# Kernel tuning notes

Measured on AMD Instinct MI355X. Metric: run time of the kernel, lower is better.

## Reference

```python
import jax, jax.numpy as jnp
from jax import lax
import numpy as np

# Config matching init_kwargs
NUM_CLASSES = 19
K = 200               # keep_k_centers
NMS_KERNEL = 9
CENTER_THR = 0.1
LABEL_DIV = 256
VOID = 255
STUFF_AREA = 4096
THING_IDS = np.array([11, 12, 13, 14, 15, 16, 17, 18])
IS_THING = jnp.zeros(NUM_CLASSES, bool).at[jnp.asarray(THING_IDS)].set(True)


def _process_one(logits, heat, offset):
    # logits [C,H,W], heat [1,H,W], offset [2,H,W]
    C, H, W = logits.shape
    sem = jnp.argmax(logits, axis=0).astype(jnp.int32)          # [H,W]
    h = heat[0]
    ht = jnp.where(h > CENTER_THR, h, 0.0)
    pad = NMS_KERNEL // 2
    # torch max_pool2d pads implicitly with -inf
    pooled = lax.reduce_window(ht, -jnp.inf, lax.max,
                               (NMS_KERNEL, NMS_KERNEL), (1, 1),
                               ((pad, pad), (pad, pad)))
    nms = jnp.where(ht == pooled, ht, 0.0)                      # [H,W]
    flat = nms.reshape(-1)
    scores, idx = lax.top_k(flat, K)                            # fixed-size center set
    valid = scores > 0.0
    num_pos = jnp.sum(flat > 0.0)
    # Match torch ordering: if more than K peaks -> topk (descending-score) order;
    # otherwise nonzero() row-major order. Invalid slots pushed to the end.
    big = jnp.int32(H * W + K)
    order_key = jnp.where(valid,
                          jnp.where(num_pos > K,
                                    jnp.arange(K, dtype=jnp.int32),
                                    idx.astype(jnp.int32)),
                          big)
    perm = jnp.argsort(order_key)
    idx = idx[perm]
    valid = valid[perm]
    FAR = 1e9  # invalid centers placed infinitely far away
    cy = jnp.where(valid, (idx // W).astype(jnp.float32), FAR)
    cx = jnp.where(valid, (idx % W).astype(jnp.float32), FAR)
    ty = jnp.arange(H, dtype=jnp.float32)[:, None] + offset[0]  # [H,W]
    tx = jnp.arange(W, dtype=jnp.float32)[None, :] + offset[1]  # [H,W]
    # squared distances [H,W,K]; argmin equals argmin of cdist
    d2 = (ty[..., None] - cy) ** 2 + (tx[..., None] - cx) ** 2
    closest = jnp.argmin(d2, axis=-1).astype(jnp.int32)         # [H,W]
    thing_mask = IS_THING[sem]
    inst = jnp.where(thing_mask & valid.any(), closest + 1, 0).astype(jnp.int32)
    # Majority class per instance via (instance, class) histogram.
    # argmax picks the smallest class among ties, matching torch.mode.
    hist = jnp.zeros((K + 1) * NUM_CLASSES, jnp.int32)
    hist = hist.at[(inst * NUM_CLASSES + sem).reshape(-1)].add(1)
    hist = hist.reshape(K + 1, NUM_CLASSES)
    majority = jnp.argmax(hist, axis=1).astype(jnp.int32)       # [K+1]
    pan = jnp.where(inst > 0, majority[inst] * LABEL_DIV + inst, VOID * LABEL_DIV)
    # Stuff: per-class pixel counts restricted to non-instance pixels
    stuff_pix = inst == 0
    skey = jnp.where(stuff_pix, sem, NUM_CLASSES).reshape(-1)
    scounts = jnp.zeros(NUM_CLASSES + 1, jnp.int32).at[skey].add(1)[:NUM_CLASSES]
    cond = stuff_pix & (~thing_mask) & (scounts[sem] >= STUFF_AREA)
    pan = jnp.where(cond, sem * LABEL_DIV, pan)
    return pan.astype(jnp.int32), inst


def setup_inputs() -> dict:
    key = jax.random.key(0)
    k1, k2, k3 = jax.random.split(key, 3)
    B, C, H, W = 2, NUM_CLASSES, 512, 1024
    semantic_logits = jax.random.normal(k1, (B, C, H, W), dtype=jnp.float32)
    center_heatmap = jax.random.uniform(k2, (B, 1, H, W), dtype=jnp.float32)
    offset_map = jax.random.normal(k3, (B, 2, H, W), dtype=jnp.float32)
    return {"semantic_logits": semantic_logits,
            "center_heatmap": center_heatmap,
            "offset_map": offset_map}


def reference(semantic_logits, center_heatmap, offset_map):
    pan, inst = jax.vmap(_process_one)(semantic_logits, center_heatmap, offset_map)
    return pan, inst
```

## Files before the change

### kernel.cpp

```cpp
#include <hip/hip_runtime.h>

#define B 2
#define C 19
#define H 512
#define W 1024
#define HW (H*W)
#define K 200
#define NCLS 19
#define HISTN ((K+1)*NCLS)
#define NT 512
#define MAXPB 128
#define SL 6912

typedef unsigned long long u64;


__global__ __launch_bounds__(256) void k_nms(const float* __restrict__ heat,
                                             u64* __restrict__ keys,
                                             int* __restrict__ pcnt) {
    __shared__ float ht[40][40];
    __shared__ float hm[40][32];
    __shared__ u64 lpk[MAXPB];
    __shared__ int lcnt;
    int b = blockIdx.z;
    int x0 = blockIdx.x * 32, y0 = blockIdx.y * 32;
    int gb = b * NT + blockIdx.y * 32 + blockIdx.x;
    int tid = threadIdx.y * 32 + threadIdx.x;
    const float* hb = heat + (size_t)b * HW;
    if (tid == 0) lcnt = 0;
    for (int i = tid; i < 40 * 40; i += 256) {
        int ly = i / 40, lx = i % 40;
        int gy = y0 + ly - 4, gx = x0 + lx - 4;
        float v = 0.f;
        if (gy >= 0 && gy < H && gx >= 0 && gx < W) {
            float hv = hb[gy * W + gx];
            v = (hv > 0.1f) ? hv : 0.f;
        }
        ht[ly][lx] = v;
    }
    __syncthreads();
    for (int i = tid; i < 40 * 32; i += 256) {
        int ly = i >> 5, lx = i & 31;
        float m = ht[ly][lx];
#pragma unroll
        for (int d = 1; d < 9; ++d) m = fmaxf(m, ht[ly][lx + d]);
        hm[ly][lx] = m;
    }
    __syncthreads();
#pragma unroll
    for (int r = 0; r < 4; ++r) {
        int oy = threadIdx.y + r * 8;
        int ox = threadIdx.x;
        float c = ht[oy + 4][ox + 4];
        if (c > 0.f) {
            float m = hm[oy][ox];
#pragma unroll
            for (int d = 1; d < 9; ++d) m = fmaxf(m, hm[oy + d][ox]);
            if (c == m) {
                int pos = atomicAdd(&lcnt, 1);
                unsigned sb = __float_as_uint(c);
                if (pos < MAXPB)
                    lpk[pos] = ((u64)(0x3F800000u - sb) << 19)
                             | (unsigned)((y0 + oy) * W + (x0 + ox));
            }
        }
    }
    __syncthreads();
    int n = (lcnt < MAXPB) ? lcnt : MAXPB;
    if (tid == 0) pcnt[gb] = n;
    for (int i = tid; i < n; i += 256)
        keys[(size_t)gb * MAXPB + i] = lpk[i];
}

__global__ __launch_bounds__(1024) void k_topk(const u64* __restrict__ keys,
                                               const int* __restrict__ pcnt,
                                               int* __restrict__ hist,
                                               int* __restrict__ anyv,
                                               float* __restrict__ cy,
                                               float* __restrict__ cx) {
    __shared__ u64 skeys[SL];
    __shared__ u64 cand[256];
    __shared__ int hcnt[256];
    __shared__ int sbase[NT], scnt[NT];
    __shared__ int wsum[16];
    __shared__ u64 s_thr;
    __shared__ int sR, gcnt, s_binc;
    int b = blockIdx.x, tid = threadIdx.x;
    int lane = tid & 63, w = tid >> 6;
    for (int i = tid; i < HISTN; i += 1024) hist[b * HISTN + i] = 0;
    int n = (tid < NT) ? pcnt[b * NT + tid] : 0;
    int incl = n;
#pragma unroll
    for (int off = 1; off < 64; off <<= 1) {
        int v = __shfl_up(incl, off, 64);
        if (lane >= off) incl += v;
    }
    if (tid < NT && lane == 63) wsum[w] = incl;
    __syncthreads();
    int N = 0;
#pragma unroll
    for (int j = 0; j < 8; ++j) N += wsum[j];
    if (tid < NT) {
        int wbase = 0;
        for (int j = 0; j < w; ++j) wbase += wsum[j];
        sbase[tid] = wbase + incl - n;
        scnt[tid] = n;
    }
    int M = (N < SL) ? N : SL;
    int Ksel = (M < K) ? M : K;
    if (tid == 0) { s_thr = 0ULL; sR = Ksel; gcnt = 0; s_binc = 0x7FFFFFFF; }
    __syncthreads();
    for (int t = w * 32; t < w * 32 + 32; ++t) {
        int nt_ = scnt[t];
        if (lane < nt_) {
            int d = sbase[t] + lane;
            if (d < SL)
                skeys[d] = keys[(size_t)(b * NT + t) * MAXPB + lane];
        }
    }
    __syncthreads();
    u64 thr;
    if (M <= K) {
        thr = ~0ULL;
    } else {
        bool donep = false;
#pragma unroll 1
        for (int d = 40; d >= 0 && !donep; d -= 8) {
            if (tid < 256) hcnt[tid] = 0;
            __syncthreads();
            u64 pref = s_thr;
            for (int i = tid; i < M; i += 1024) {
                u64 kk = skeys[i];
                if ((kk >> (d + 8)) == (pref >> (d + 8)))
                    atomicAdd(&hcnt[(int)((kk >> d) & 255ULL)], 1);
            }
            __syncthreads();
            if (tid < 64) {
                int h0 = hcnt[tid * 4 + 0], h1 = hcnt[tid * 4 + 1];
                int h2 = hcnt[tid * 4 + 2], h3 = hcnt[tid * 4 + 3];
                int s = h0 + h1 + h2 + h3;
                int ic = s;
#pragma unroll
                for (int off = 1; off < 64; off <<= 1) {
                    int v = __shfl_up(ic, off, 64);
                    if (tid >= off) ic += v;
                }
                int R = sR;
                int before = ic - s;
                if (before < R && R <= ic) {
                    int c = before, t = tid * 4;
                    if (c + h0 < R) { c += h0; t++;
                        if (c + h1 < R) { c += h1; t++;
                            if (c + h2 < R) { c += h2; t++; } } }
                    s_thr = pref | ((u64)t << d);
                    sR = R - c;
                    s_binc = hcnt[t];
                }
            }
            __syncthreads();
            if (s_binc <= 256) {
                u64 p2 = s_thr;
                for (int i = tid; i < M; i += 1024) {
                    u64 kk = skeys[i];
                    if ((kk >> d) == (p2 >> d)) {
                        int p = atomicAdd(&gcnt, 1);
                        if (p < 256) cand[p] = kk;
                    }
                }
                __syncthreads();
                int g = (gcnt < 256) ? gcnt : 256;
                if (tid < g) {
                    u64 v = cand[tid];
                    int r = 0;
                    for (int j = 0; j < g; ++j) r += (int)(cand[j] < v);
                    if (r == sR - 1) s_thr = v;
                }
                __syncthreads();
                if (tid == 0) gcnt = 0;
                donep = true;
                __syncthreads();
            }
        }
        thr = s_thr;
    }
    for (int i = tid; i < M; i += 1024) {
        u64 kk = skeys[i];
        if (kk <= thr) {
            int p = atomicAdd(&gcnt, 1);
            if (p < 256) cand[p] = kk;
        }
    }
    __syncthreads();
    if (tid < 256) {
        int g = (gcnt < 256) ? gcnt : 256;
        u64 v = (tid < g) ? cand[tid] : ~0ULL;
        if (N <= K && tid < g) v &= 0x7FFFFULL;
        cand[tid] = v;
    }
    __syncthreads();
    if (tid < 256) {
        u64 v = cand[tid];
        int r = 0;
#pragma unroll 8
        for (int j = 0; j < 256; ++j) {
            u64 cj = cand[j];
            r += (int)((cj < v) || (cj == v && j < tid));
        }
        skeys[r] = v;
    }
    __syncthreads();
    if (tid < K) {
        bool valid = tid < Ksel;
        unsigned idx = (unsigned)(skeys[tid] & 0x7FFFFULL);
        cy[b * K + tid] = valid ? (float)(idx >> 10) : 1e9f;
        cx[b * K + tid] = valid ? (float)(idx & 1023) : 1e9f;
    }
    if (tid == 0) anyv[b] = (N > 0) ? 1 : 0;
}

__global__ __launch_bounds__(256) void k_inst(const float* __restrict__ logits,
                                              const float* __restrict__ offs,
                                              const float* __restrict__ gcy,
                                              const float* __restrict__ gcx,
                                              const int* __restrict__ anyv,
                                              int* __restrict__ packed,
                                              int* __restrict__ hist) {
    __shared__ int lh[HISTN];
    __shared__ float scy[K], scx[K];
    __shared__ unsigned char skk[K];
    __shared__ float red[4][8];
    __shared__ int wcnt[4];
    int b = blockIdx.z;
    int x0 = blockIdx.x << 5, y0 = blockIdx.y << 5;
    int tid = threadIdx.x;
    int lane = tid & 63, w = tid >> 6;
    for (int i = tid; i < HISTN; i += 256) lh[i] = 0;
    int r = tid >> 3;
    int c0 = (tid & 7) << 2;
    int gy = y0 + r;
    int gxb = x0 + c0;
    int q = (gy << 10) + gxb;
    const float* ob = offs + (size_t)b * 2 * HW;
    float4 oy4 = *(const float4*)(ob + q);
    float4 ox4 = *(const float4*)(ob + HW + q);
    int av = anyv[b];
    const float4* l4 = (const float4*)(logits + (size_t)b * C * HW) + (q >> 2);
    float4 vv[C];
#pragma unroll
    for (int c = 0; c < C; ++c) vv[c] = l4[(size_t)c * (HW / 4)];
    float fy = (float)gy, fx = (float)gxb;
    float ty[4] = {fy + oy4.x, fy + oy4.y, fy + oy4.z, fy + oy4.w};
    float tx[4] = {fx + ox4.x, fx + 1.f + ox4.y, fx + 2.f + ox4.z, fx + 3.f + ox4.w};
    float tylo = fminf(fminf(ty[0], ty[1]), fminf(ty[2], ty[3]));
    float tyhi = fmaxf(fmaxf(ty[0], ty[1]), fmaxf(ty[2], ty[3]));
    float txlo = fminf(fminf(tx[0], tx[1]), fminf(tx[2], tx[3]));
    float txhi = fmaxf(fmaxf(tx[0], tx[1]), fmaxf(tx[2], tx[3]));
#pragma unroll
    for (int off = 32; off; off >>= 1) {
        tylo = fminf(tylo, __shfl_xor(tylo, off, 64));
        tyhi = fmaxf(tyhi, __shfl_xor(tyhi, off, 64));
        txlo = fminf(txlo, __shfl_xor(txlo, off, 64));
        txhi = fmaxf(txhi, __shfl_xor(txhi, off, 64));
    }
    if (lane == 0) { red[w][0] = tylo; red[w][1] = tyhi; red[w][2] = txlo; red[w][3] = txhi; }
    __syncthreads();
    tylo = fminf(fminf(red[0][0], red[1][0]), fminf(red[2][0], red[3][0]));
    tyhi = fmaxf(fmaxf(red[0][1], red[1][1]), fmaxf(red[2][1], red[3][1]));
    txlo = fminf(fminf(red[0][2], red[1][2]), fminf(red[2][2], red[3][2]));
    txhi = fmaxf(fmaxf(red[0][3], red[1][3]), fmaxf(red[2][3], red[3][3]));
    float kcy = 0.f, kcx = 0.f, mind2 = 0.f, maxd2 = 3.4e38f;
    if (tid < K) {
        kcy = gcy[b * K + tid]; kcx = gcx[b * K + tid];
        float dmy = fmaxf(fmaxf(tylo - kcy, kcy - tyhi), 0.f);
        float dMy = fmaxf(tyhi - kcy, kcy - tylo);
        float dmx = fmaxf(fmaxf(txlo - kcx, kcx - txhi), 0.f);
        float dMx = fmaxf(txhi - kcx, kcx - txlo);
        mind2 = dmy * dmy + dmx * dmx;
        maxd2 = dMy * dMy + dMx * dMx;
    }
    float mv = maxd2;
#pragma unroll
    for (int off = 32; off; off >>= 1) mv = fminf(mv, __shfl_xor(mv, off, 64));
    if (lane == 0) red[w][4] = mv;
    __syncthreads();
    float m = fminf(fminf(red[0][4], red[1][4]), fminf(red[2][4], red[3][4]));
    bool keep = (tid < K) && (mind2 <= m * 1.0001f + 1.0f);
    u64 bal = __ballot(keep);
    if (lane == 0) wcnt[w] = (int)__popcll(bal);
    __syncthreads();
    int nk = wcnt[0] + wcnt[1] + wcnt[2] + wcnt[3];
    if (keep) {
        int base = (w > 0 ? wcnt[0] : 0) + (w > 1 ? wcnt[1] : 0) + (w > 2 ? wcnt[2] : 0);
        int rank = base + (int)__popcll(bal & ((1ULL << lane) - 1ULL));
        scy[rank] = kcy; scx[rank] = kcx; skk[rank] = (unsigned char)tid;
    }
    float best[4] = {vv[0].x, vv[0].y, vv[0].z, vv[0].w};
    int bc[4] = {0, 0, 0, 0};
#pragma unroll
    for (int c = 1; c < C; ++c) {
        if (vv[c].x > best[0]) { best[0] = vv[c].x; bc[0] = c; }
        if (vv[c].y > best[1]) { best[1] = vv[c].y; bc[1] = c; }
        if (vv[c].z > best[2]) { best[2] = vv[c].z; bc[2] = c; }
        if (vv[c].w > best[3]) { best[3] = vv[c].w; bc[3] = c; }
    }
    __syncthreads();
    float bd[4] = {3.4e38f, 3.4e38f, 3.4e38f, 3.4e38f};
    int bi[4] = {0, 0, 0, 0};
    if (av) {
        for (int i = 0; i < nk; ++i) {
            float cyk = scy[i], cxk = scx[i];
#pragma unroll
            for (int j = 0; j < 4; ++j) {
                float dy = __fsub_rn(ty[j], cyk);
                float dx = __fsub_rn(tx[j], cxk);
                float d2 = __fadd_rn(__fmul_rn(dy, dy), __fmul_rn(dx, dx));
                if (d2 < bd[j]) { bd[j] = d2; bi[j] = i; }
            }
        }
    }
    int4 pk4;
    int* pkp = (int*)&pk4;
#pragma unroll
    for (int j = 0; j < 4; ++j) {
        int s = bc[j];
        int ins = (s >= 11 && av) ? ((int)skk[bi[j]] + 1) : 0;
        pkp[j] = (s << 8) | ins;
        atomicAdd(&lh[ins * NCLS + s], 1);
    }
    *(int4*)(packed + b * HW + q) = pk4;
    __syncthreads();
    for (int i = tid; i < HISTN; i += 256)
        if (lh[i]) atomicAdd(&hist[b * HISTN + i], lh[i]);
}

__global__ __launch_bounds__(256) void k_pan(int* __restrict__ pansem,
                                             int* __restrict__ inst,
                                             const int* __restrict__ hist) {
    __shared__ int lh[HISTN];
    __shared__ unsigned char maj[K + 1];
    int b = blockIdx.x >> 8;
    int blk = blockIdx.x & 255;
    int tid = threadIdx.x;
    const int* hb = hist + b * HISTN;
    for (int i = tid; i < HISTN; i += 256) lh[i] = hb[i];
    __syncthreads();
    if (tid <= K) {
        const int* h = &lh[tid * NCLS];
        int best = h[0], bc = 0;
#pragma unroll
        for (int c = 1; c < NCLS; ++c)
            if (h[c] > best) { best = h[c]; bc = c; }
        maj[tid] = (unsigned char)bc;
    }
    __syncthreads();
    int p0 = b * HW + blk * 2048;
    const int4* s4 = (const int4*)(pansem + p0);
    int4 pka = s4[tid * 2], pkb = s4[tid * 2 + 1];
    int4 pa, pb, ia, ib;
    int* kp = (int*)&pka; int* pp = (int*)&pa; int* ip = (int*)&ia;
#pragma unroll
    for (int j = 0; j < 4; ++j) {
        int s = kp[j] >> 8, in_ = kp[j] & 255;
        pp[j] = (in_ > 0) ? ((int)maj[in_] * 256 + in_)
               : ((s < 11 && lh[s] >= 4096) ? s * 256 : 65280);
        ip[j] = in_;
    }
    kp = (int*)&pkb; pp = (int*)&pb; ip = (int*)&ib;
#pragma unroll
    for (int j = 0; j < 4; ++j) {
        int s = kp[j] >> 8, in_ = kp[j] & 255;
        pp[j] = (in_ > 0) ? ((int)maj[in_] * 256 + in_)
               : ((s < 11 && lh[s] >= 4096) ? s * 256 : 65280);
        ip[j] = in_;
    }
    ((int4*)(pansem + p0))[tid * 2] = pa;
    ((int4*)(pansem + p0))[tid * 2 + 1] = pb;
    ((int4*)(inst + p0))[tid * 2] = ia;
    ((int4*)(inst + p0))[tid * 2 + 1] = ib;
}

extern "C" void kernel_launch(void* const* d_in, const int* in_sizes, int n_in,
                              void* d_out, int out_size, void* d_ws, size_t ws_size,
                              hipStream_t stream) {
    const float* logits = (const float*)d_in[0];
    const float* heat   = (const float*)d_in[1];
    const float* offs   = (const float*)d_in[2];
    int* out = (int*)d_out;
    int* pansem = out;
    int* inst = out + B * HW;
    int* wsi = (int*)d_ws;
    int* hist = wsi + 16;
    float* cy = (float*)(wsi + 8192);
    float* cx = cy + B * K;
    int* pcnt = wsi + 9216;
    int* anyv = wsi + 10496;
    u64* keys = (u64*)((char*)d_ws + 65536);

    k_nms<<<dim3(32, 16, B), dim3(32, 8, 1), 0, stream>>>(heat, keys, pcnt);
    k_topk<<<B, 1024, 0, stream>>>(keys, pcnt, hist, anyv, cy, cx);
    k_inst<<<dim3(32, 16, B), 256, 0, stream>>>(logits, offs, cy, cx, anyv, pansem, hist);
    k_pan<<<B * 256, 256, 0, stream>>>(pansem, inst, hist);
}
```

Before: 75.52 us.

## Shrink k_inst tiles to 32x16 and restructure top-k key gather

The instance kernel now has each thread handle 2 pixels instead of 4 and covers 32x16 tiles, which doubles the grid. The aim is more blocks in flight and lower register pressure, and the smaller tiles should also give tighter center-pruning bounds. In exchange, the per-block pruning and histogram-flush overhead doubles. Separately, MAXPB drops from 128 to 64 peaks per NMS tile, and the top-k gather uses one prefix array with strided tile ownership per wave. A tile with more than 64 peaks would now be truncated.

Measured after the change: 83.50 us. 1.11x slower.

```diff
diff --git a/kernel.cpp b/kernel.cpp
--- a/kernel.cpp
+++ b/kernel.cpp
@@ -9,7 +9,7 @@
 #define NCLS 19
 #define HISTN ((K+1)*NCLS)
 #define NT 512
-#define MAXPB 128
+#define MAXPB 64
 #define SL 6912
 
 typedef unsigned long long u64;
@@ -81,8 +81,8 @@
     __shared__ u64 skeys[SL];
     __shared__ u64 cand[256];
     __shared__ int hcnt[256];
-    __shared__ int sbase[NT], scnt[NT];
-    __shared__ int wsum[16];
+    __shared__ int sbase[NT + 1];
+    __shared__ int wsum[8];
     __shared__ u64 s_thr;
     __shared__ int sR, gcnt, s_binc;
     int b = blockIdx.x, tid = threadIdx.x;
@@ -104,18 +104,23 @@
         int wbase = 0;
         for (int j = 0; j < w; ++j) wbase += wsum[j];
         sbase[tid] = wbase + incl - n;
-        scnt[tid] = n;
+        if (tid == NT - 1) sbase[NT] = N;
     }
     int M = (N < SL) ? N : SL;
     int Ksel = (M < K) ? M : K;
     if (tid == 0) { s_thr = 0ULL; sR = Ksel; gcnt = 0; s_binc = 0x7FFFFFFF; }
     __syncthreads();
-    for (int t = w * 32; t < w * 32 + 32; ++t) {
-        int nt_ = scnt[t];
-        if (lane < nt_) {
-            int d = sbase[t] + lane;
-            if (d < SL)
-                skeys[d] = keys[(size_t)(b * NT + t) * MAXPB + lane];
+    {
+        int t = w;
+        const u64* kb = keys + (size_t)b * NT * MAXPB;
+#pragma unroll 1
+        for (int it = 0; it < NT / 16; ++it, t += 16) {
+            int base = sbase[t];
+            int cnt_ = sbase[t + 1] - base;
+            if (lane < cnt_) {
+                int d = base + lane;
+                if (d < SL) skeys[d] = kb[(size_t)t * MAXPB + lane];
+            }
         }
     }
     __syncthreads();
@@ -231,30 +236,28 @@
     __shared__ float red[4][8];
     __shared__ int wcnt[4];
     int b = blockIdx.z;
-    int x0 = blockIdx.x << 5, y0 = blockIdx.y << 5;
+    int x0 = blockIdx.x << 5, y0 = blockIdx.y << 4;
     int tid = threadIdx.x;
     int lane = tid & 63, w = tid >> 6;
     for (int i = tid; i < HISTN; i += 256) lh[i] = 0;
-    int r = tid >> 3;
-    int c0 = (tid & 7) << 2;
+    int r = tid >> 4;
+    int c0 = (tid & 15) << 1;
     int gy = y0 + r;
     int gxb = x0 + c0;
     int q = (gy << 10) + gxb;
     const float* ob = offs + (size_t)b * 2 * HW;
-    float4 oy4 = *(const float4*)(ob + q);
-    float4 ox4 = *(const float4*)(ob + HW + q);
+    float2 oy2 = *(const float2*)(ob + q);
+    float2 ox2 = *(const float2*)(ob + HW + q);
     int av = anyv[b];
-    const float4* l4 = (const float4*)(logits + (size_t)b * C * HW) + (q >> 2);
-    float4 vv[C];
-#pragma unroll
-    for (int c = 0; c < C; ++c) vv[c] = l4[(size_t)c * (HW / 4)];
+    const float2* l2 = (const float2*)(logits + (size_t)b * C * HW) + (q >> 1);
+    float2 vv[C];
+#pragma unroll
+    for (int c = 0; c < C; ++c) vv[c] = l2[(size_t)c * (HW / 2)];
     float fy = (float)gy, fx = (float)gxb;
-    float ty[4] = {fy + oy4.x, fy + oy4.y, fy + oy4.z, fy + oy4.w};
-    float tx[4] = {fx + ox4.x, fx + 1.f + ox4.y, fx + 2.f + ox4.z, fx + 3.f + ox4.w};
-    float tylo = fminf(fminf(ty[0], ty[1]), fminf(ty[2], ty[3]));
-    float tyhi = fmaxf(fmaxf(ty[0], ty[1]), fmaxf(ty[2], ty[3]));
-    float txlo = fminf(fminf(tx[0], tx[1]), fminf(tx[2], tx[3]));
-    float txhi = fmaxf(fmaxf(tx[0], tx[1]), fmaxf(tx[2], tx[3]));
+    float ty[2] = {fy + oy2.x, fy + oy2.y};
+    float tx[2] = {fx + ox2.x, fx + 1.f + ox2.y};
+    float tylo = fminf(ty[0], ty[1]), tyhi = fmaxf(ty[0], ty[1]);
+    float txlo = fminf(tx[0], tx[1]), txhi = fmaxf(tx[0], tx[1]);
 #pragma unroll
     for (int off = 32; off; off >>= 1) {
         tylo = fminf(tylo, __shfl_xor(tylo, off, 64));
@@ -294,23 +297,21 @@
         int rank = base + (int)__popcll(bal & ((1ULL << lane) - 1ULL));
         scy[rank] = kcy; scx[rank] = kcx; skk[rank] = (unsigned char)tid;
     }
-    float best[4] = {vv[0].x, vv[0].y, vv[0].z, vv[0].w};
-    int bc[4] = {0, 0, 0, 0};
+    float best[2] = {vv[0].x, vv[0].y};
+    int bc[2] = {0, 0};
 #pragma unroll
     for (int c = 1; c < C; ++c) {
         if (vv[c].x > best[0]) { best[0] = vv[c].x; bc[0] = c; }
         if (vv[c].y > best[1]) { best[1] = vv[c].y; bc[1] = c; }
-        if (vv[c].z > best[2]) { best[2] = vv[c].z; bc[2] = c; }
-        if (vv[c].w > best[3]) { best[3] = vv[c].w; bc[3] = c; }
-    }
-    __syncthreads();
-    float bd[4] = {3.4e38f, 3.4e38f, 3.4e38f, 3.4e38f};
-    int bi[4] = {0, 0, 0, 0};
+    }
+    __syncthreads();
+    float bd[2] = {3.4e38f, 3.4e38f};
+    int bi[2] = {0, 0};
     if (av) {
         for (int i = 0; i < nk; ++i) {
             float cyk = scy[i], cxk = scx[i];
 #pragma unroll
-            for (int j = 0; j < 4; ++j) {
+            for (int j = 0; j < 2; ++j) {
                 float dy = __fsub_rn(ty[j], cyk);
                 float dx = __fsub_rn(tx[j], cxk);
                 float d2 = __fadd_rn(__fmul_rn(dy, dy), __fmul_rn(dx, dx));
@@ -318,16 +319,16 @@
             }
         }
     }
-    int4 pk4;
-    int* pkp = (int*)&pk4;
-#pragma unroll
-    for (int j = 0; j < 4; ++j) {
+    int2 pk2;
+    int* pkp = (int*)&pk2;
+#pragma unroll
+    for (int j = 0; j < 2; ++j) {
         int s = bc[j];
         int ins = (s >= 11 && av) ? ((int)skk[bi[j]] + 1) : 0;
         pkp[j] = (s << 8) | ins;
         atomicAdd(&lh[ins * NCLS + s], 1);
     }
-    *(int4*)(packed + b * HW + q) = pk4;
+    *(int2*)(packed + b * HW + q) = pk2;
     __syncthreads();
     for (int i = tid; i < HISTN; i += 256)
         if (lh[i]) atomicAdd(&hist[b * HISTN + i], lh[i]);
@@ -398,6 +399,6 @@
 
     k_nms<<<dim3(32, 16, B), dim3(32, 8, 1), 0, stream>>>(heat, keys, pcnt);
     k_topk<<<B, 1024, 0, stream>>>(keys, pcnt, hist, anyv, cy, cx);
-    k_inst<<<dim3(32, 16, B), 256, 0, stream>>>(logits, offs, cy, cx, anyv, pansem, hist);
+    k_inst<<<dim3(32, 32, B), 256, 0, stream>>>(logits, offs, cy, cx, anyv, pansem, hist);
     k_pan<<<B * 256, 256, 0, stream>>>(pansem, inst, hist);
 }
```

## Split semantic argmax into a separate kernel and compact top-k key gathering

Applied to the files above, without the earlier changes.

Moves the 19-class argmax out of the instance kernel into a standalone k_sem kernel that writes the class into the packed buffer, which the renamed k_ctr kernel then reads back. The intent is to lighten register pressure and raise occupancy in the center-assignment kernel, and to let the logits read run as a plain streaming pass. The cost is an extra launch plus an extra write and read of the packed buffer. It also halves MAXPB (per-block peak capacity) and rewrites the topk gather loop to use a prefix-sum array, which risks dropping peaks if a block has more than 64.

Result: slower. 79.48 us (+5.2%).

```diff
diff --git a/kernel.cpp b/kernel.cpp
--- a/kernel.cpp
+++ b/kernel.cpp
@@ -9,11 +9,34 @@
 #define NCLS 19
 #define HISTN ((K+1)*NCLS)
 #define NT 512
-#define MAXPB 128
+#define MAXPB 64
 #define SL 6912
 
 typedef unsigned long long u64;
 
+
+__global__ __launch_bounds__(256) void k_sem(const float* __restrict__ logits,
+                                             int* __restrict__ packed) {
+    int p = blockIdx.x * 256 + threadIdx.x;
+    int b = p >> 17;
+    int q4 = p & 131071;
+    const float4* l4 = (const float4*)(logits + (size_t)b * C * HW) + q4;
+    float4 vv[C];
+#pragma unroll
+    for (int c = 0; c < C; ++c) vv[c] = l4[(size_t)c * (HW / 4)];
+    float best[4] = {vv[0].x, vv[0].y, vv[0].z, vv[0].w};
+    int bc[4] = {0, 0, 0, 0};
+#pragma unroll
+    for (int c = 1; c < C; ++c) {
+        if (vv[c].x > best[0]) { best[0] = vv[c].x; bc[0] = c; }
+        if (vv[c].y > best[1]) { best[1] = vv[c].y; bc[1] = c; }
+        if (vv[c].z > best[2]) { best[2] = vv[c].z; bc[2] = c; }
+        if (vv[c].w > best[3]) { best[3] = vv[c].w; bc[3] = c; }
+    }
+    int4 pk4;
+    pk4.x = bc[0] << 8; pk4.y = bc[1] << 8; pk4.z = bc[2] << 8; pk4.w = bc[3] << 8;
+    ((int4*)packed)[p] = pk4;
+}
 
 __global__ __launch_bounds__(256) void k_nms(const float* __restrict__ heat,
                                              u64* __restrict__ keys,
@@ -81,8 +104,8 @@
     __shared__ u64 skeys[SL];
     __shared__ u64 cand[256];
     __shared__ int hcnt[256];
-    __shared__ int sbase[NT], scnt[NT];
-    __shared__ int wsum[16];
+    __shared__ int sbase[NT + 1];
+    __shared__ int wsum[8];
     __shared__ u64 s_thr;
     __shared__ int sR, gcnt, s_binc;
     int b = blockIdx.x, tid = threadIdx.x;
@@ -104,18 +127,23 @@
         int wbase = 0;
         for (int j = 0; j < w; ++j) wbase += wsum[j];
         sbase[tid] = wbase + incl - n;
-        scnt[tid] = n;
+        if (tid == NT - 1) sbase[NT] = N;
     }
     int M = (N < SL) ? N : SL;
     int Ksel = (M < K) ? M : K;
     if (tid == 0) { s_thr = 0ULL; sR = Ksel; gcnt = 0; s_binc = 0x7FFFFFFF; }
     __syncthreads();
-    for (int t = w * 32; t < w * 32 + 32; ++t) {
-        int nt_ = scnt[t];
-        if (lane < nt_) {
-            int d = sbase[t] + lane;
-            if (d < SL)
-                skeys[d] = keys[(size_t)(b * NT + t) * MAXPB + lane];
+    {
+        int t = w;
+        const u64* kb = keys + (size_t)b * NT * MAXPB;
+#pragma unroll 1
+        for (int it = 0; it < NT / 16; ++it, t += 16) {
+            int base = sbase[t];
+            int cnt_ = sbase[t + 1] - base;
+            if (lane < cnt_) {
+                int d = base + lane;
+                if (d < SL) skeys[d] = kb[(size_t)t * MAXPB + lane];
+            }
         }
     }
     __syncthreads();
@@ -218,13 +246,12 @@
     if (tid == 0) anyv[b] = (N > 0) ? 1 : 0;
 }
 
-__global__ __launch_bounds__(256) void k_inst(const float* __restrict__ logits,
-                                              const float* __restrict__ offs,
-                                              const float* __restrict__ gcy,
-                                              const float* __restrict__ gcx,
-                                              const int* __restrict__ anyv,
-                                              int* __restrict__ packed,
-                                              int* __restrict__ hist) {
+__global__ __launch_bounds__(256) void k_ctr(const float* __restrict__ offs,
+                                             const float* __restrict__ gcy,
+                                             const float* __restrict__ gcx,
+                                             const int* __restrict__ anyv,
+                                             int* __restrict__ packed,
+                                             int* __restrict__ hist) {
     __shared__ int lh[HISTN];
     __shared__ float scy[K], scx[K];
     __shared__ unsigned char skk[K];
@@ -243,11 +270,8 @@
     const float* ob = offs + (size_t)b * 2 * HW;
     float4 oy4 = *(const float4*)(ob + q);
     float4 ox4 = *(const float4*)(ob + HW + q);
+    int4 pk4 = *(const int4*)(packed + b * HW + q);
     int av = anyv[b];
-    const float4* l4 = (const float4*)(logits + (size_t)b * C * HW) + (q >> 2);
-    float4 vv[C];
-#pragma unroll
-    for (int c = 0; c < C; ++c) vv[c] = l4[(size_t)c * (HW / 4)];
     float fy = (float)gy, fx = (float)gxb;
     float ty[4] = {fy + oy4.x, fy + oy4.y, fy + oy4.z, fy + oy4.w};
     float tx[4] = {fx + ox4.x, fx + 1.f + ox4.y, fx + 2.f + ox4.z, fx + 3.f + ox4.w};
@@ -294,15 +318,6 @@
         int rank = base + (int)__popcll(bal & ((1ULL << lane) - 1ULL));
         scy[rank] = kcy; scx[rank] = kcx; skk[rank] = (unsigned char)tid;
     }
-    float best[4] = {vv[0].x, vv[0].y, vv[0].z, vv[0].w};
-    int bc[4] = {0, 0, 0, 0};
-#pragma unroll
-    for (int c = 1; c < C; ++c) {
-        if (vv[c].x > best[0]) { best[0] = vv[c].x; bc[0] = c; }
-        if (vv[c].y > best[1]) { best[1] = vv[c].y; bc[1] = c; }
-        if (vv[c].z > best[2]) { best[2] = vv[c].z; bc[2] = c; }
-        if (vv[c].w > best[3]) { best[3] = vv[c].w; bc[3] = c; }
-    }
     __syncthreads();
     float bd[4] = {3.4e38f, 3.4e38f, 3.4e38f, 3.4e38f};
     int bi[4] = {0, 0, 0, 0};
@@ -318,11 +333,10 @@
             }
         }
     }
-    int4 pk4;
     int* pkp = (int*)&pk4;
 #pragma unroll
     for (int j = 0; j < 4; ++j) {
-        int s = bc[j];
+        int s = pkp[j] >> 8;
         int ins = (s >= 11 && av) ? ((int)skk[bi[j]] + 1) : 0;
         pkp[j] = (s << 8) | ins;
         atomicAdd(&lh[ins * NCLS + s], 1);
@@ -396,8 +410,9 @@
     int* anyv = wsi + 10496;
     u64* keys = (u64*)((char*)d_ws + 65536);
 
+    k_sem<<<B * HW / 4 / 256, 256, 0, stream>>>(logits, pansem);
     k_nms<<<dim3(32, 16, B), dim3(32, 8, 1), 0, stream>>>(heat, keys, pcnt);
     k_topk<<<B, 1024, 0, stream>>>(keys, pcnt, hist, anyv, cy, cx);
-    k_inst<<<dim3(32, 16, B), 256, 0, stream>>>(logits, offs, cy, cx, anyv, pansem, hist);
+    k_ctr<<<dim3(32, 16, B), 256, 0, stream>>>(offs, cy, cx, anyv, pansem, hist);
     k_pan<<<B * 256, 256, 0, stream>>>(pansem, inst, hist);
 }
```
